# Kernel optimization log

Measured on AMD Instinct MI355X. Metric: run time of the kernel, lower is better.

Reference implementation:

```python
import jax, jax.numpy as jnp
import numpy as np

N_NODES = 50000
N_EDGES = 800000
FEAT_DIM = 16
HIDDEN = 128
N_LAYERS = 4
OUT_DIM = 12
N_GRAPHS = 1024

def setup_inputs() -> dict:
    key = jax.random.key(0)
    ks = jax.random.split(key, 8)
    return {
        "x": jax.random.normal(ks[0], (N_NODES, FEAT_DIM), jnp.float32),
        "edge_index": jax.random.randint(ks[1], (2, N_EDGES), 0, N_NODES, dtype=jnp.int32),
        "edge_attr": jnp.zeros((N_EDGES, 4), jnp.float32),
        "batch_idx": jnp.sort(jax.random.randint(ks[2], (N_NODES,), 0, N_GRAPHS, dtype=jnp.int32)),
        # node-embed MLP: Linear(16,128) -> relu -> Linear(128,128)
        "W_e1": jax.random.normal(ks[3], (FEAT_DIM, HIDDEN), jnp.float32) * 0.1,
        "b_e1": jnp.zeros((HIDDEN,), jnp.float32),
        "W_e2": jax.random.normal(ks[4], (HIDDEN, HIDDEN), jnp.float32) * 0.05,
        "b_e2": jnp.zeros((HIDDEN,), jnp.float32),
        # stacked GCNConv weights/biases for 4 layers
        "W_g": jax.random.normal(ks[5], (N_LAYERS, HIDDEN, HIDDEN), jnp.float32) * 0.05,
        "b_g": jnp.zeros((N_LAYERS, HIDDEN), jnp.float32),
        # output Linear(128,12)
        "W_o": jax.random.normal(ks[6], (HIDDEN, OUT_DIM), jnp.float32) * 0.05,
        "b_o": jnp.zeros((OUT_DIM,), jnp.float32),
    }

def _gcn_layer(h_in, src, dst, W, b):
    # PyG GCNConv with add_self_loops=True, symmetric normalization:
    # out_i = sum_{j in N(i) u {i}} (d_i d_j)^{-1/2} (x_j W) + b
    h = h_in @ W                                   # [N, H]
    deg = jnp.zeros((N_NODES,), h.dtype).at[dst].add(1.0) + 1.0  # +1 self-loop
    dinv = jax.lax.rsqrt(deg)                      # [N]
    norm = dinv[src] * dinv[dst]                   # [E]
    msg = h[src] * norm[:, None]                   # gather + scale  [E, H]
    agg = jnp.zeros_like(h).at[dst].add(msg)       # scatter-add to targets
    agg = agg + h * (dinv * dinv)[:, None]         # self-loop term
    return agg + b

def reference(x, edge_index, edge_attr, batch_idx, W_e1, b_e1, W_e2, b_e2, W_g, b_g, W_o, b_o):
    del edge_attr  # use_edge_attribution=False; GCNConv ignores edge features
    src, dst = edge_index[0], edge_index[1]
    # node embedding MLP
    h = jax.nn.relu(x @ W_e1 + b_e1) @ W_e2 + b_e2
    for i in range(N_LAYERS):
        h = jax.nn.relu(_gcn_layer(h, src, dst, W_g[i], b_g[i]))
        # dropout is identity in eval mode
    # scatter-mean pooling over graphs
    sums = jax.ops.segment_sum(h, batch_idx, num_segments=N_GRAPHS)
    cnts = jax.ops.segment_sum(jnp.ones((N_NODES,), h.dtype), batch_idx, num_segments=N_GRAPHS)
    pooled = sums / jnp.maximum(cnts, 1.0)[:, None]
    return pooled @ W_o + b_o
```

## Files before the change

kernel.cpp:

```cpp
#include <hip/hip_runtime.h>

#define N_NODES 50000
#define N_EDGES 800000
#define FEAT    16
#define HID     128
#define NLAYERS 4
#define OUTD    12
#define NGRAPH  1024
#define SCAN_NB 196

__device__ inline float4 f4zero() { return make_float4(0.f, 0.f, 0.f, 0.f); }
__device__ inline float4 f4fma(float a, float4 w, float4 acc) {
    acc.x = fmaf(a, w.x, acc.x);
    acc.y = fmaf(a, w.y, acc.y);
    acc.z = fmaf(a, w.z, acc.z);
    acc.w = fmaf(a, w.w, acc.w);
    return acc;
}
__device__ inline float4 f4add(float4 a, float4 b) {
    return make_float4(a.x + b.x, a.y + b.y, a.z + b.z, a.w + b.w);
}
__device__ inline float4 f4relu(float4 a) {
    return make_float4(fmaxf(a.x, 0.f), fmaxf(a.y, 0.f), fmaxf(a.z, 0.f), fmaxf(a.w, 0.f));
}

__global__ void k_deg(const int* __restrict__ ei, int* __restrict__ degi) {
    int e = blockIdx.x * 256 + threadIdx.x;
    if (e < N_EDGES) atomicAdd(&degi[ei[N_EDGES + e]], 1);
}

__global__ void k_dinv(const int* __restrict__ degi, float* __restrict__ dinv) {
    int i = blockIdx.x * 256 + threadIdx.x;
    if (i < N_NODES) dinv[i] = rsqrtf((float)degi[i] + 1.0f);
}

__global__ void k_scan_part(const int* __restrict__ degi, int* __restrict__ part) {
    __shared__ int s[256];
    int t = threadIdx.x;
    int i = blockIdx.x * 256 + t;
    int v = (i < N_NODES) ? degi[i] : 0;
    s[t] = v;
    __syncthreads();
    for (int st = 128; st > 0; st >>= 1) {
        if (t < st) s[t] += s[t + st];
        __syncthreads();
    }
    if (t == 0) part[blockIdx.x] = s[0];
}

__global__ void k_scan_mid(int* __restrict__ part) {
    __shared__ int s[256];
    int t = threadIdx.x;
    int v = (t < SCAN_NB) ? part[t] : 0;
    s[t] = v;
    __syncthreads();
    for (int st = 1; st < 256; st <<= 1) {
        int u = (t >= st) ? s[t - st] : 0;
        __syncthreads();
        s[t] += u;
        __syncthreads();
    }
    if (t < SCAN_NB) part[t] = s[t] - v;
}

__global__ void k_scan_final(const int* __restrict__ degi, const int* __restrict__ part,
                             int* __restrict__ offs) {
    __shared__ int s[256];
    int t = threadIdx.x;
    int i = blockIdx.x * 256 + t;
    int v = (i < N_NODES) ? degi[i] : 0;
    s[t] = v;
    __syncthreads();
    for (int st = 1; st < 256; st <<= 1) {
        int u = (t >= st) ? s[t - st] : 0;
        __syncthreads();
        s[t] += u;
        __syncthreads();
    }
    if (i <= N_NODES) offs[i] = s[t] - v + part[blockIdx.x];
}

__global__ void k_fill(const int* __restrict__ ei, const int* __restrict__ offs,
                       const float* __restrict__ dinv,
                       int* __restrict__ cursor, int2* __restrict__ erec) {
    int e = blockIdx.x * 256 + threadIdx.x;
    if (e < N_EDGES) {
        int srcv = ei[e];
        int dstv = ei[N_EDGES + e];
        int p = atomicAdd(&cursor[dstv], 1);
        erec[offs[dstv] + p] = make_int2(srcv, __float_as_int(dinv[srcv]));
    }
}

#define GM 64
__global__ void __launch_bounds__(256) k_embed_fused(
        const float* __restrict__ x,
        const float* __restrict__ W1, const float* __restrict__ b1,
        const float* __restrict__ W2, const float* __restrict__ b2,
        float* __restrict__ outp) {
    __shared__ float x_l[GM][FEAT];
    __shared__ float a_l[GM][HID];
    int t = threadIdx.x;
    long n0 = (long)blockIdx.x * GM;
    {
        int r  = t >> 2;
        int c4 = (t & 3) << 2;
        long n = n0 + r;
        float4 v = (n < N_NODES) ? *(const float4*)&x[n * FEAT + c4] : f4zero();
        *(float4*)&x_l[r][c4] = v;
    }
    __syncthreads();
    int fgrp = t & 31, ngrp = t >> 5;
    int f4 = fgrp << 2;
    {
        float4 acc[8];
#pragma unroll
        for (int r = 0; r < 8; ++r) acc[r] = f4zero();
#pragma unroll
        for (int k4 = 0; k4 < 4; ++k4) {
            float4 wv[4];
#pragma unroll
            for (int kk = 0; kk < 4; ++kk)
                wv[kk] = *(const float4*)&W1[(k4 * 4 + kk) * HID + f4];
            float4 xv[8];
#pragma unroll
            for (int r = 0; r < 8; ++r)
                xv[r] = *(const float4*)&x_l[ngrp * 8 + r][k4 << 2];
#pragma unroll
            for (int r = 0; r < 8; ++r) {
                acc[r] = f4fma(xv[r].x, wv[0], acc[r]);
                acc[r] = f4fma(xv[r].y, wv[1], acc[r]);
                acc[r] = f4fma(xv[r].z, wv[2], acc[r]);
                acc[r] = f4fma(xv[r].w, wv[3], acc[r]);
            }
        }
        float4 bv = *(const float4*)&b1[f4];
#pragma unroll
        for (int r = 0; r < 8; ++r)
            *(float4*)&a_l[ngrp * 8 + r][f4] = f4relu(f4add(acc[r], bv));
    }
    __syncthreads();
    float4 acc[8];
#pragma unroll
    for (int r = 0; r < 8; ++r) acc[r] = f4zero();
#pragma unroll 4
    for (int k4 = 0; k4 < 32; ++k4) {
        float4 wv[4];
#pragma unroll
        for (int kk = 0; kk < 4; ++kk)
            wv[kk] = *(const float4*)&W2[(k4 * 4 + kk) * HID + f4];
        float4 av[8];
#pragma unroll
        for (int r = 0; r < 8; ++r)
            av[r] = *(const float4*)&a_l[ngrp * 8 + r][k4 << 2];
#pragma unroll
        for (int r = 0; r < 8; ++r) {
            acc[r] = f4fma(av[r].x, wv[0], acc[r]);
            acc[r] = f4fma(av[r].y, wv[1], acc[r]);
            acc[r] = f4fma(av[r].z, wv[2], acc[r]);
            acc[r] = f4fma(av[r].w, wv[3], acc[r]);
        }
    }
    float4 bv = *(const float4*)&b2[f4];
#pragma unroll
    for (int r = 0; r < 8; ++r) {
        long n = n0 + ngrp * 8 + r;
        if (n < N_NODES) *(float4*)&outp[n * HID + f4] = f4add(acc[r], bv);
    }
}

__global__ void __launch_bounds__(256) k_gemm(
        const float* __restrict__ A, const float* __restrict__ W,
        float* __restrict__ B) {
    __shared__ float a_l[GM][HID];
    int t = threadIdx.x;
    long n0 = (long)blockIdx.x * GM;
#pragma unroll
    for (int i = 0; i < 8; ++i) {
        int p  = t + 256 * i;
        int r  = p >> 5;
        int c4 = (p & 31) << 2;
        long n = n0 + r;
        float4 v = (n < N_NODES) ? *(const float4*)&A[n * HID + c4] : f4zero();
        *(float4*)&a_l[r][c4] = v;
    }
    __syncthreads();
    int fgrp = t & 31, ngrp = t >> 5;
    int f4 = fgrp << 2;
    float4 acc[8];
#pragma unroll
    for (int r = 0; r < 8; ++r) acc[r] = f4zero();
#pragma unroll 4
    for (int k4 = 0; k4 < 32; ++k4) {
        float4 wv[4];
#pragma unroll
        for (int kk = 0; kk < 4; ++kk)
            wv[kk] = *(const float4*)&W[(k4 * 4 + kk) * HID + f4];
        float4 av[8];
#pragma unroll
        for (int r = 0; r < 8; ++r)
            av[r] = *(const float4*)&a_l[ngrp * 8 + r][k4 << 2];
#pragma unroll
        for (int r = 0; r < 8; ++r) {
            acc[r] = f4fma(av[r].x, wv[0], acc[r]);
            acc[r] = f4fma(av[r].y, wv[1], acc[r]);
            acc[r] = f4fma(av[r].z, wv[2], acc[r]);
            acc[r] = f4fma(av[r].w, wv[3], acc[r]);
        }
    }
#pragma unroll
    for (int r = 0; r < 8; ++r) {
        long n = n0 + ngrp * 8 + r;
        if (n < N_NODES) *(float4*)&B[n * HID + f4] = acc[r];
    }
}

__global__ void __launch_bounds__(256) k_agg(
        const float* __restrict__ hp,
        const int2* __restrict__ erec, const int* __restrict__ offs,
        const float* __restrict__ dinv, const float* __restrict__ bias,
        float* __restrict__ hout) {
    int t = threadIdx.x;
    int lane = t & 63;
    int w = t >> 6;
    int i = blockIdx.x * 4 + w;
    if (i >= N_NODES) return;
    float di = dinv[i];
    int s0 = offs[i], s1 = offs[i + 1];
    const float2* hp2 = (const float2*)hp;
    float2 self = hp2[(long)i * 64 + lane];
    float2 bv = ((const float2*)bias)[lane];
    float ax = fmaf(di * di, self.x, bv.x);
    float ay = fmaf(di * di, self.y, bv.y);
    for (int base = s0; base < s1; base += 64) {
        int n = s1 - base; if (n > 64) n = 64;
        int last = n - 1;
        int2 e = (lane < n) ? erec[base + lane] : make_int2(0, 0);
        int   sv_l = e.x;
        float nm_l = __int_as_float(e.y);
        for (int k = 0; k < n; k += 16) {
            int a[16]; float m[16];
#pragma unroll
            for (int u = 0; u < 16; ++u) {
                int kk = k + u;
                int ks = kk < last ? kk : last;
                a[u] = __shfl(sv_l, ks);
                float mu = __shfl(nm_l, ks);
                m[u] = (kk < n) ? mu * di : 0.f;
            }
            float2 v[16];
#pragma unroll
            for (int u = 0; u < 16; ++u) v[u] = hp2[(long)a[u] * 64 + lane];
#pragma unroll
            for (int u = 0; u < 16; ++u) {
                ax = fmaf(m[u], v[u].x, ax);
                ay = fmaf(m[u], v[u].y, ay);
            }
        }
    }
    float2 r;
    r.x = fmaxf(ax, 0.f);
    r.y = fmaxf(ay, 0.f);
    ((float2*)hout)[(long)i * 64 + lane] = r;
}

#define PN 16
__global__ void __launch_bounds__(256) k_pool(
        const float* __restrict__ h, const int* __restrict__ batch,
        float* __restrict__ pooled, float* __restrict__ cnt) {
    int t = threadIdx.x;
    int lane = t & 31, grp = t >> 5;
    long n0 = ((long)blockIdx.x * 8 + grp) * PN;
    if (n0 >= N_NODES) return;
    long n1 = n0 + PN; if (n1 > N_NODES) n1 = N_NODES;
    const float4* h4 = (const float4*)h;
    float4 run = f4zero();
    int curg = batch[n0];
    int c = 0;
    for (long n = n0; n < n1; ++n) {
        int g = batch[n];
        if (g != curg) {
            float* pb = &pooled[(long)curg * HID + (lane << 2)];
            atomicAdd(pb + 0, run.x); atomicAdd(pb + 1, run.y);
            atomicAdd(pb + 2, run.z); atomicAdd(pb + 3, run.w);
            if (lane == 0) atomicAdd(&cnt[curg], (float)c);
            run = f4zero(); c = 0; curg = g;
        }
        run = f4add(run, h4[n * 32 + lane]);
        ++c;
    }
    float* pb = &pooled[(long)curg * HID + (lane << 2)];
    atomicAdd(pb + 0, run.x); atomicAdd(pb + 1, run.y);
    atomicAdd(pb + 2, run.z); atomicAdd(pb + 3, run.w);
    if (lane == 0) atomicAdd(&cnt[curg], (float)c);
}

__global__ void __launch_bounds__(HID) k_out(
        const float* __restrict__ pooled, const float* __restrict__ cnt,
        const float* __restrict__ Wo, const float* __restrict__ bo,
        float* __restrict__ out) {
    __shared__ float p[HID];
    int g = blockIdx.x;
    int f = threadIdx.x;
    float inv = 1.0f / fmaxf(cnt[g], 1.0f);
    p[f] = pooled[g * HID + f] * inv;
    __syncthreads();
    if (f < OUTD) {
        float acc = bo[f];
#pragma unroll 8
        for (int k = 0; k < HID; ++k) acc += p[k] * Wo[k * OUTD + f];
        out[g * OUTD + f] = acc;
    }
}

extern "C" void kernel_launch(void* const* d_in, const int* in_sizes, int n_in,
                              void* d_out, int out_size, void* d_ws, size_t ws_size,
                              hipStream_t stream) {
    const float* x    = (const float*)d_in[0];
    const int*   ei   = (const int*)d_in[1];
    const int*   bidx = (const int*)d_in[3];
    const float* We1  = (const float*)d_in[4];
    const float* be1  = (const float*)d_in[5];
    const float* We2  = (const float*)d_in[6];
    const float* be2  = (const float*)d_in[7];
    const float* Wg   = (const float*)d_in[8];
    const float* bg   = (const float*)d_in[9];
    const float* Wo   = (const float*)d_in[10];
    const float* bo   = (const float*)d_in[11];
    float* out = (float*)d_out;

    char* ws = (char*)d_ws;
    size_t o = 0;
    auto take = [&](size_t bytes) { size_t r = o; o += (bytes + 255) & ~(size_t)255; return r; };
    size_t off_degi   = take((size_t)N_NODES * 4);
    size_t off_cursor = take((size_t)N_NODES * 4);
    size_t off_pooled = take((size_t)NGRAPH * HID * 4);
    size_t off_cnt    = take((size_t)NGRAPH * 4);
    size_t zero_bytes = o;
    size_t off_dinv   = take((size_t)N_NODES * 4);
    size_t off_offs   = take((size_t)(N_NODES + 1) * 4);
    size_t off_part   = take((size_t)256 * 4);
    size_t off_erec   = take((size_t)N_EDGES * 8);
    size_t off_hA     = take((size_t)N_NODES * HID * 4);
    size_t off_hB     = take((size_t)N_NODES * HID * 4);

    int*   degi   = (int*)(ws + off_degi);
    int*   cursor = (int*)(ws + off_cursor);
    float* pooled = (float*)(ws + off_pooled);
    float* cnt    = (float*)(ws + off_cnt);
    float* dinv   = (float*)(ws + off_dinv);
    int*   offs   = (int*)(ws + off_offs);
    int*   part   = (int*)(ws + off_part);
    int2*  erec   = (int2*)(ws + off_erec);
    float* hA     = (float*)(ws + off_hA);
    float* hB     = (float*)(ws + off_hB);

    hipMemsetAsync(d_ws, 0, zero_bytes, stream);

    k_deg<<<(N_EDGES + 255) / 256, 256, 0, stream>>>(ei, degi);
    k_dinv<<<(N_NODES + 255) / 256, 256, 0, stream>>>(degi, dinv);
    k_scan_part<<<SCAN_NB, 256, 0, stream>>>(degi, part);
    k_scan_mid<<<1, 256, 0, stream>>>(part);
    k_scan_final<<<SCAN_NB, 256, 0, stream>>>(degi, part, offs);
    k_fill<<<(N_EDGES + 255) / 256, 256, 0, stream>>>(ei, offs, dinv, cursor, erec);

    int gemm_grid = (N_NODES + GM - 1) / GM;
    k_embed_fused<<<gemm_grid, 256, 0, stream>>>(x, We1, be1, We2, be2, hA);

    for (int l = 0; l < NLAYERS; ++l) {
        k_gemm<<<gemm_grid, 256, 0, stream>>>(hA, Wg + (size_t)l * HID * HID, hB);
        k_agg<<<(N_NODES + 3) / 4, 256, 0, stream>>>(hB, erec, offs, dinv,
                                                     bg + (size_t)l * HID, hA);
    }

    k_pool<<<(N_NODES + 8 * PN - 1) / (8 * PN), 256, 0, stream>>>(hA, bidx, pooled, cnt);
    k_out<<<NGRAPH, HID, 0, stream>>>(pooled, cnt, Wo, bo, out);
}
```

Measured before the change: 601.9 us.

## Fuse GCN aggregation and GEMM into one per-tile layer kernel

Reorders each GCN layer to aggregate first, (A·h)·W instead of A·(h·W), and fuses the gather-aggregate with the dense GEMM, bias and ReLU in a single kernel. Aggregated rows go straight into shared memory, which removes the intermediate hB write and read and one launch per layer. The cost is much less parallelism in the latency-bound gather phase: each block has only 4 waves, each walking 16 nodes serially, and the gather unroll drops from 16 to 8. That may hurt the memory-level parallelism of the irregular gathers.

After: 579.8 us. 1.04x faster.

```diff
diff --git a/kernel.cpp b/kernel.cpp
--- a/kernel.cpp
+++ b/kernel.cpp
@@ -169,22 +169,60 @@
     }
 }
 
-__global__ void __launch_bounds__(256) k_gemm(
-        const float* __restrict__ A, const float* __restrict__ W,
-        float* __restrict__ B) {
+__global__ void __launch_bounds__(256) k_layer(
+        const float* __restrict__ h,
+        const int2* __restrict__ erec, const int* __restrict__ offs,
+        const float* __restrict__ dinv,
+        const float* __restrict__ W, const float* __restrict__ bias,
+        float* __restrict__ hout) {
     __shared__ float a_l[GM][HID];
     int t = threadIdx.x;
+    int lane = t & 63;
+    int w = t >> 6;
     long n0 = (long)blockIdx.x * GM;
-#pragma unroll
-    for (int i = 0; i < 8; ++i) {
-        int p  = t + 256 * i;
-        int r  = p >> 5;
-        int c4 = (p & 31) << 2;
-        long n = n0 + r;
-        float4 v = (n < N_NODES) ? *(const float4*)&A[n * HID + c4] : f4zero();
-        *(float4*)&a_l[r][c4] = v;
-    }
-    __syncthreads();
+    const float2* h2 = (const float2*)h;
+
+    for (int rep = 0; rep < 16; ++rep) {
+        int row = w * 16 + rep;
+        long i = n0 + row;
+        float ax = 0.f, ay = 0.f;
+        if (i < N_NODES) {
+            float di = dinv[i];
+            int s0 = offs[i], s1 = offs[i + 1];
+            float2 self = h2[i * 64 + lane];
+            ax = di * di * self.x;
+            ay = di * di * self.y;
+            for (int base = s0; base < s1; base += 64) {
+                int n = s1 - base; if (n > 64) n = 64;
+                int last = n - 1;
+                int2 e = (lane < n) ? erec[base + lane] : make_int2(0, 0);
+                int   sv_l = e.x;
+                float nm_l = __int_as_float(e.y);
+                for (int k = 0; k < n; k += 8) {
+                    int a[8]; float m[8];
+#pragma unroll
+                    for (int u = 0; u < 8; ++u) {
+                        int kk = k + u;
+                        int ks = kk < last ? kk : last;
+                        a[u] = __shfl(sv_l, ks);
+                        float mu = __shfl(nm_l, ks);
+                        m[u] = (kk < n) ? mu * di : 0.f;
+                    }
+                    float2 v[8];
+#pragma unroll
+                    for (int u = 0; u < 8; ++u) v[u] = h2[(long)a[u] * 64 + lane];
+#pragma unroll
+                    for (int u = 0; u < 8; ++u) {
+                        ax = fmaf(m[u], v[u].x, ax);
+                        ay = fmaf(m[u], v[u].y, ay);
+                    }
+                }
+            }
+        }
+        *(float2*)&a_l[row][lane << 1] = make_float2(ax, ay);
+    }
+    __syncthreads();
+
     int fgrp = t & 31, ngrp = t >> 5;
     int f4 = fgrp << 2;
     float4 acc[8];
@@ -208,60 +246,12 @@
             acc[r] = f4fma(av[r].w, wv[3], acc[r]);
         }
     }
+    float4 bv = *(const float4*)&bias[f4];
 #pragma unroll
     for (int r = 0; r < 8; ++r) {
         long n = n0 + ngrp * 8 + r;
-        if (n < N_NODES) *(float4*)&B[n * HID + f4] = acc[r];
-    }
-}
-
-__global__ void __launch_bounds__(256) k_agg(
-        const float* __restrict__ hp,
-        const int2* __restrict__ erec, const int* __restrict__ offs,
-        const float* __restrict__ dinv, const float* __restrict__ bias,
-        float* __restrict__ hout) {
-    int t = threadIdx.x;
-    int lane = t & 63;
-    int w = t >> 6;
-    int i = blockIdx.x * 4 + w;
-    if (i >= N_NODES) return;
-    float di = dinv[i];
-    int s0 = offs[i], s1 = offs[i + 1];
-    const float2* hp2 = (const float2*)hp;
-    float2 self = hp2[(long)i * 64 + lane];
-    float2 bv = ((const float2*)bias)[lane];
-    float ax = fmaf(di * di, self.x, bv.x);
-    float ay = fmaf(di * di, self.y, bv.y);
-    for (int base = s0; base < s1; base += 64) {
-        int n = s1 - base; if (n > 64) n = 64;
-        int last = n - 1;
-        int2 e = (lane < n) ? erec[base + lane] : make_int2(0, 0);
-        int   sv_l = e.x;
-        float nm_l = __int_as_float(e.y);
-        for (int k = 0; k < n; k += 16) {
-            int a[16]; float m[16];
-#pragma unroll
-            for (int u = 0; u < 16; ++u) {
-                int kk = k + u;
-                int ks = kk < last ? kk : last;
-                a[u] = __shfl(sv_l, ks);
-                float mu = __shfl(nm_l, ks);
-                m[u] = (kk < n) ? mu * di : 0.f;
-            }
-            float2 v[16];
-#pragma unroll
-            for (int u = 0; u < 16; ++u) v[u] = hp2[(long)a[u] * 64 + lane];
-#pragma unroll
-            for (int u = 0; u < 16; ++u) {
-                ax = fmaf(m[u], v[u].x, ax);
-                ay = fmaf(m[u], v[u].y, ay);
-            }
-        }
-    }
-    float2 r;
-    r.x = fmaxf(ax, 0.f);
-    r.y = fmaxf(ay, 0.f);
-    ((float2*)hout)[(long)i * 64 + lane] = r;
+        if (n < N_NODES) *(float4*)&hout[n * HID + f4] = f4relu(f4add(acc[r], bv));
+    }
 }
 
 #define PN 16
@@ -364,15 +354,18 @@
     k_scan_final<<<SCAN_NB, 256, 0, stream>>>(degi, part, offs);
     k_fill<<<(N_EDGES + 255) / 256, 256, 0, stream>>>(ei, offs, dinv, cursor, erec);
 
-    int gemm_grid = (N_NODES + GM - 1) / GM;
-    k_embed_fused<<<gemm_grid, 256, 0, stream>>>(x, We1, be1, We2, be2, hA);
-
+    int tile_grid = (N_NODES + GM - 1) / GM;
+    k_embed_fused<<<tile_grid, 256, 0, stream>>>(x, We1, be1, We2, be2, hA);
+
+    float* hin = hA;
+    float* hout2 = hB;
     for (int l = 0; l < NLAYERS; ++l) {
-        k_gemm<<<gemm_grid, 256, 0, stream>>>(hA, Wg + (size_t)l * HID * HID, hB);
-        k_agg<<<(N_NODES + 3) / 4, 256, 0, stream>>>(hB, erec, offs, dinv,
-                                                     bg + (size_t)l * HID, hA);
-    }
-
-    k_pool<<<(N_NODES + 8 * PN - 1) / (8 * PN), 256, 0, stream>>>(hA, bidx, pooled, cnt);
+        k_layer<<<tile_grid, 256, 0, stream>>>(hin, erec, offs, dinv,
+                                               Wg + (size_t)l * HID * HID,
+                                               bg + (size_t)l * HID, hout2);
+        float* tmp = hin; hin = hout2; hout2 = tmp;
+    }
+
+    k_pool<<<(N_NODES + 8 * PN - 1) / (8 * PN), 256, 0, stream>>>(hin, bidx, pooled, cnt);
     k_out<<<NGRAPH, HID, 0, stream>>>(pooled, cnt, Wo, bo, out);
 }
```

## Slice GEMM output by feature and aggregate per slice for cache locality

Applied to the files above, without the earlier changes.

The GEMM now writes its output in a sliced layout, eight slices of 16 features each stored contiguously per node, using nontemporal stores. A new aggregation kernel gives each block one feature slice and a chunk of nodes. Each wavefront handles 16 edges at a time, with 4 lanes per edge, and reduces across lanes with xor shuffles. The aim is to shrink the gathered working set per slice to 3.2MB so the random neighbour gathers hit in L2, at the price of reading the edge lists eight times and adding shuffle reductions.

Result: slower. 959.7 us (+59.5%).

```diff
diff --git a/kernel.cpp b/kernel.cpp
--- a/kernel.cpp
+++ b/kernel.cpp
@@ -8,6 +8,10 @@
 #define OUTD    12
 #define NGRAPH  1024
 #define SCAN_NB 196
+#define SLICES  8
+#define SLICE_F 16
+
+typedef float f32x4 __attribute__((ext_vector_type(4)));
 
 __device__ inline float4 f4zero() { return make_float4(0.f, 0.f, 0.f, 0.f); }
 __device__ inline float4 f4fma(float a, float4 w, float4 acc) {
@@ -22,6 +26,10 @@
 }
 __device__ inline float4 f4relu(float4 a) {
     return make_float4(fmaxf(a.x, 0.f), fmaxf(a.y, 0.f), fmaxf(a.z, 0.f), fmaxf(a.w, 0.f));
+}
+__device__ inline void nt_store_f4(float4 v, float4* p) {
+    f32x4 nv; nv.x = v.x; nv.y = v.y; nv.z = v.z; nv.w = v.w;
+    __builtin_nontemporal_store(nv, (f32x4*)p);
 }
 
 __global__ void k_deg(const int* __restrict__ ei, int* __restrict__ degi) {
@@ -171,7 +179,7 @@
 
 __global__ void __launch_bounds__(256) k_gemm(
         const float* __restrict__ A, const float* __restrict__ W,
-        float* __restrict__ B) {
+        float4* __restrict__ Bs) {
     __shared__ float a_l[GM][HID];
     int t = threadIdx.x;
     long n0 = (long)blockIdx.x * GM;
@@ -208,60 +216,59 @@
             acc[r] = f4fma(av[r].w, wv[3], acc[r]);
         }
     }
+    int s = fgrp >> 2, c = fgrp & 3;
 #pragma unroll
     for (int r = 0; r < 8; ++r) {
         long n = n0 + ngrp * 8 + r;
-        if (n < N_NODES) *(float4*)&B[n * HID + f4] = acc[r];
-    }
-}
-
-__global__ void __launch_bounds__(256) k_agg(
-        const float* __restrict__ hp,
-        const int2* __restrict__ erec, const int* __restrict__ offs,
-        const float* __restrict__ dinv, const float* __restrict__ bias,
-        float* __restrict__ hout) {
-    int t = threadIdx.x;
-    int lane = t & 63;
-    int w = t >> 6;
-    int i = blockIdx.x * 4 + w;
-    if (i >= N_NODES) return;
-    float di = dinv[i];
-    int s0 = offs[i], s1 = offs[i + 1];
-    const float2* hp2 = (const float2*)hp;
-    float2 self = hp2[(long)i * 64 + lane];
-    float2 bv = ((const float2*)bias)[lane];
-    float ax = fmaf(di * di, self.x, bv.x);
-    float ay = fmaf(di * di, self.y, bv.y);
-    for (int base = s0; base < s1; base += 64) {
-        int n = s1 - base; if (n > 64) n = 64;
-        int last = n - 1;
-        int2 e = (lane < n) ? erec[base + lane] : make_int2(0, 0);
-        int   sv_l = e.x;
-        float nm_l = __int_as_float(e.y);
-        for (int k = 0; k < n; k += 16) {
-            int a[16]; float m[16];
-#pragma unroll
-            for (int u = 0; u < 16; ++u) {
-                int kk = k + u;
-                int ks = kk < last ? kk : last;
-                a[u] = __shfl(sv_l, ks);
-                float mu = __shfl(nm_l, ks);
-                m[u] = (kk < n) ? mu * di : 0.f;
-            }
-            float2 v[16];
-#pragma unroll
-            for (int u = 0; u < 16; ++u) v[u] = hp2[(long)a[u] * 64 + lane];
-#pragma unroll
-            for (int u = 0; u < 16; ++u) {
-                ax = fmaf(m[u], v[u].x, ax);
-                ay = fmaf(m[u], v[u].y, ay);
-            }
-        }
-    }
-    float2 r;
-    r.x = fmaxf(ax, 0.f);
-    r.y = fmaxf(ay, 0.f);
-    ((float2*)hout)[(long)i * 64 + lane] = r;
+        if (n < N_NODES)
+            nt_store_f4(acc[r], &Bs[((long)s * N_NODES + n) * 4 + c]);
+    }
+}
+
+__global__ void __launch_bounds__(256) k_aggs(
+        const float4* __restrict__ Bs, const long long* __restrict__ erec,
+        const int* __restrict__ offs, const float* __restrict__ dinv,
+        const float* __restrict__ bias, float* __restrict__ hout) {
+    int t = threadIdx.x;
+    int lane = t & 63, w = t >> 6;
+    int s = blockIdx.x & 7;
+    int chunk = blockIdx.x >> 3;
+    const float4* sb = Bs + (long)s * N_NODES * 4;
+    int eg = lane >> 2, c = lane & 3;
+    float4 bv = *(const float4*)&bias[s * SLICE_F + (c << 2)];
+    for (int rep = 0; rep < 16; ++rep) {
+        long i = (long)chunk * 64 + w * 16 + rep;
+        if (i >= N_NODES) break;
+        float di = dinv[i];
+        int s0 = offs[i], s1 = offs[i + 1];
+        float4 acc = f4zero();
+        if (eg == 0) {
+            float4 sv4 = sb[i * 4 + c];
+            float dd = di * di;
+            acc.x = dd * sv4.x; acc.y = dd * sv4.y;
+            acc.z = dd * sv4.z; acc.w = dd * sv4.w;
+        }
+        for (int b = s0; b < s1; b += 16) {
+            int n = s1 - b; if (n > 16) n = 16;
+            long long ev = (lane < n) ? __builtin_nontemporal_load(&erec[b + lane]) : 0LL;
+            long long ee = __shfl(ev, eg);
+            int   sv = (int)(ee & 0xffffffffLL);
+            float nm = (eg < n) ? __int_as_float((int)(ee >> 32)) * di : 0.f;
+            float4 v = sb[(long)sv * 4 + c];
+            acc = f4fma(nm, v, acc);
+        }
+#pragma unroll
+        for (int m = 4; m <= 32; m <<= 1) {
+            acc.x += __shfl_xor(acc.x, m);
+            acc.y += __shfl_xor(acc.y, m);
+            acc.z += __shfl_xor(acc.z, m);
+            acc.w += __shfl_xor(acc.w, m);
+        }
+        if (lane < 4) {
+            float4 r = f4relu(f4add(acc, bv));
+            nt_store_f4(r, (float4*)&hout[i * HID + s * SLICE_F] + lane);
+        }
+    }
 }
 
 #define PN 16
@@ -353,7 +360,7 @@
     int*   part   = (int*)(ws + off_part);
     int2*  erec   = (int2*)(ws + off_erec);
     float* hA     = (float*)(ws + off_hA);
-    float* hB     = (float*)(ws + off_hB);
+    float4* Bs    = (float4*)(ws + off_hB);
 
     hipMemsetAsync(d_ws, 0, zero_bytes, stream);
 
@@ -364,13 +371,14 @@
     k_scan_final<<<SCAN_NB, 256, 0, stream>>>(degi, part, offs);
     k_fill<<<(N_EDGES + 255) / 256, 256, 0, stream>>>(ei, offs, dinv, cursor, erec);
 
-    int gemm_grid = (N_NODES + GM - 1) / GM;
-    k_embed_fused<<<gemm_grid, 256, 0, stream>>>(x, We1, be1, We2, be2, hA);
-
+    int tile_grid = (N_NODES + GM - 1) / GM;
+    k_embed_fused<<<tile_grid, 256, 0, stream>>>(x, We1, be1, We2, be2, hA);
+
+    int agg_grid = ((N_NODES + 63) / 64) * SLICES;
     for (int l = 0; l < NLAYERS; ++l) {
-        k_gemm<<<gemm_grid, 256, 0, stream>>>(hA, Wg + (size_t)l * HID * HID, hB);
-        k_agg<<<(N_NODES + 3) / 4, 256, 0, stream>>>(hB, erec, offs, dinv,
-                                                     bg + (size_t)l * HID, hA);
+        k_gemm<<<tile_grid, 256, 0, stream>>>(hA, Wg + (size_t)l * HID * HID, Bs);
+        k_aggs<<<agg_grid, 256, 0, stream>>>(Bs, (const long long*)erec, offs, dinv,
+                                             bg + (size_t)l * HID, hA);
     }
 
     k_pool<<<(N_NODES + 8 * PN - 1) / (8 * PN), 256, 0, stream>>>(hA, bidx, pooled, cnt);
```
